# Performance work log

Hardware: AMD Instinct MI355X
Metric: run time of the kernel (lower is better)

## Reference

```python
import jax, jax.numpy as jnp
import numpy as np


def _gskan_layer(x, Lam, eps, a):
    # x: [B, n_in], Lam: [n_in, n_out], eps: [n_out], a: scalar PReLU weight
    s = x[:, :, None] + eps  # [B, n_in, n_out] broadcast add
    act = jnp.where(s >= 0, s, a * s)  # PReLU with single shared parameter
    return jnp.einsum('bpq,pq->bq', act, Lam)  # weighted sum over n_in


def setup_inputs() -> dict:
    key = jax.random.key(0)
    B, input_dim, width, depth, output_dim = 1024, 256, 512, 3, 256
    dims = [input_dim] + [width] * depth + [output_dim]
    ks = jax.random.split(key, 1 + 2 * (len(dims) - 1))
    inp = {"x": jax.random.normal(ks[0], (B, input_dim), dtype=jnp.float32)}
    for i in range(len(dims) - 1):
        n_in, n_out = dims[i], dims[i + 1]
        inp[f"L{i}_Lambda"] = 0.02 * jax.random.normal(ks[1 + 2 * i], (n_in, n_out), dtype=jnp.float32)
        inp[f"L{i}_eps"] = 0.02 * jax.random.normal(ks[2 + 2 * i], (n_out,), dtype=jnp.float32)
        inp[f"L{i}_a"] = jnp.float32(0.25)  # PReLU default init
    return inp


def reference(x,
              L0_Lambda, L0_eps, L0_a,
              L1_Lambda, L1_eps, L1_a,
              L2_Lambda, L2_eps, L2_a,
              L3_Lambda, L3_eps, L3_a):
    params = [(L0_Lambda, L0_eps, L0_a), (L1_Lambda, L1_eps, L1_a),
              (L2_Lambda, L2_eps, L2_a), (L3_Lambda, L3_eps, L3_a)]
    for Lam, eps, a in params:
        x = _gskan_layer(x, Lam, eps, a)
    return x
```

## Files before the change

### kernel.cpp

```cpp
#include <hip/hip_runtime.h>


#define PCHUNK 32
#define XS_STRIDE 36

__global__ __launch_bounds__(256) void gskan_partial_kernel(
    const float* __restrict__ X,
    const float* __restrict__ Lam,
    const float* __restrict__ Eps,
    const float* __restrict__ Aw,
    float* __restrict__ Part,
    int B, int n_in, int n_out, int p_per_split)
{
    __shared__ float xs[64 * XS_STRIDE];
    __shared__ float ls[PCHUNK * 64];

    const int tid = threadIdx.x;
    const int qg  = tid & 15;
    const int bl  = tid >> 4;

    const int q0 = blockIdx.x * 64;
    const int b0 = blockIdx.y * 64;
    const int p_begin = blockIdx.z * p_per_split;
    int p_end = p_begin + p_per_split;
    if (p_end > n_in) p_end = n_in;

    const float a  = Aw[0];
    const float c1 = 0.5f * (1.0f + a);
    const float c2 = 0.5f * (1.0f - a);

    const float4 ev = *reinterpret_cast<const float4*>(Eps + q0 + qg * 4);
    const float ee[4] = {ev.x, ev.y, ev.z, ev.w};

    float acc1[4][4] = {};
    float acc2[4][4] = {};

    for (int pc = p_begin; pc < p_end; pc += PCHUNK) {
        #pragma unroll
        for (int r = 0; r < 2; ++r) {
            int slot = r * 256 + tid;
            int row  = slot >> 3;
            int pg   = slot & 7;
            float4 v = *reinterpret_cast<const float4*>(
                X + (size_t)(b0 + row) * n_in + pc + pg * 4);
            *reinterpret_cast<float4*>(&xs[row * XS_STRIDE + pg * 4]) = v;
        }
        #pragma unroll
        for (int r = 0; r < 2; ++r) {
            int slot = r * 256 + tid;
            int row  = slot >> 4;
            int c4   = slot & 15;
            float4 v = *reinterpret_cast<const float4*>(
                Lam + (size_t)(pc + row) * n_out + q0 + c4 * 4);
            *reinterpret_cast<float4*>(&ls[row * 64 + c4 * 4]) = v;
        }
        __syncthreads();

        #pragma unroll
        for (int p = 0; p < PCHUNK; p += 4) {
            float4 xv[4];
            #pragma unroll
            for (int i = 0; i < 4; ++i)
                xv[i] = *reinterpret_cast<const float4*>(&xs[(bl * 4 + i) * XS_STRIDE + p]);

            #pragma unroll
            for (int pp = 0; pp < 4; ++pp) {
                float4 lv = *reinterpret_cast<const float4*>(&ls[(p + pp) * 64 + qg * 4]);
                const float le[4] = {lv.x, lv.y, lv.z, lv.w};
                #pragma unroll
                for (int i = 0; i < 4; ++i) {
                    const float xe = (pp == 0) ? xv[i].x :
                                     (pp == 1) ? xv[i].y :
                                     (pp == 2) ? xv[i].z : xv[i].w;
                    #pragma unroll
                    for (int j = 0; j < 4; ++j) {
                        const float s = xe + ee[j];
                        acc1[i][j] = fmaf(s,        le[j], acc1[i][j]);
                        acc2[i][j] = fmaf(fabsf(s), le[j], acc2[i][j]);
                    }
                }
            }
        }
        __syncthreads();
    }

    float* P = Part + (size_t)blockIdx.z * B * n_out;
    #pragma unroll
    for (int i = 0; i < 4; ++i) {
        const int b = b0 + bl * 4 + i;
        float4 o;
        o.x = c1 * acc1[i][0] + c2 * acc2[i][0];
        o.y = c1 * acc1[i][1] + c2 * acc2[i][1];
        o.z = c1 * acc1[i][2] + c2 * acc2[i][2];
        o.w = c1 * acc1[i][3] + c2 * acc2[i][3];
        *reinterpret_cast<float4*>(P + (size_t)b * n_out + q0 + qg * 4) = o;
    }
}

__global__ __launch_bounds__(256) void gskan_combine_kernel(
    const float* __restrict__ Part, float* __restrict__ Y, int n, int nsplit)
{
    int i = (blockIdx.x * 256 + threadIdx.x) * 4;
    if (i >= n) return;
    float4 acc = *reinterpret_cast<const float4*>(Part + i);
    for (int s = 1; s < nsplit; ++s) {
        float4 v = *reinterpret_cast<const float4*>(Part + (size_t)s * n + i);
        acc.x += v.x; acc.y += v.y; acc.z += v.z; acc.w += v.w;
    }
    *reinterpret_cast<float4*>(Y + i) = acc;
}

extern "C" void kernel_launch(void* const* d_in, const int* in_sizes, int n_in_args,
                              void* d_out, int out_size, void* d_ws, size_t ws_size,
                              hipStream_t stream)
{
    (void)n_in_args; (void)out_size;

    const float* x = (const float*)d_in[0];

    struct LayerP { const float *Lam, *Eps, *Aw; int n_in, n_out; };
    LayerP layers[4];
    for (int i = 0; i < 4; ++i) {
        layers[i].Lam   = (const float*)d_in[1 + 3 * i];
        layers[i].Eps   = (const float*)d_in[2 + 3 * i];
        layers[i].Aw    = (const float*)d_in[3 + 3 * i];
        layers[i].n_out = in_sizes[2 + 3 * i];
        layers[i].n_in  = in_sizes[1 + 3 * i] / layers[i].n_out;
    }
    const int B = in_sizes[0] / layers[0].n_in;

    char* ws = (char*)d_ws;
    float* Part = (float*)ws;
    float* yA   = (float*)(ws + (size_t)(16u << 20));
    float* yB   = (float*)(ws + (size_t)(18u << 20));
    const bool have_ws = ws_size >= (size_t)(20u << 20);

    const float* cur = x;
    for (int i = 0; i < 4; ++i) {
        const LayerP& ly = layers[i];
        const int nq = ly.n_out / 64;
        const int nb = B / 64;

        int nsplit = 1;
        if (have_ws) {
            nsplit = 1024 / (nq * nb);
            if (nsplit < 1) nsplit = 1;
            int max_split = ly.n_in / PCHUNK;
            if (nsplit > max_split) nsplit = max_split;
        }
        int p_per = ((ly.n_in + nsplit * PCHUNK - 1) / (nsplit * PCHUNK)) * PCHUNK;
        nsplit = (ly.n_in + p_per - 1) / p_per;

        while ((size_t)nsplit * B * ly.n_out * 4 > ((size_t)16u << 20)) nsplit--;
        if (nsplit < 1) nsplit = 1;
        p_per = ((ly.n_in + nsplit * PCHUNK - 1) / (nsplit * PCHUNK)) * PCHUNK;
        nsplit = (ly.n_in + p_per - 1) / p_per;

        float* Y = (i == 3) ? (float*)d_out : ((i % 2 == 0) ? yA : yB);
        float* dst = (nsplit == 1) ? Y : Part;

        dim3 grid(nq, nb, nsplit), block(256);
        hipLaunchKernelGGL(gskan_partial_kernel, grid, block, 0, stream,
                           cur, ly.Lam, ly.Eps, ly.Aw, dst,
                           B, ly.n_in, ly.n_out, p_per);

        if (nsplit > 1) {
            const int n = B * ly.n_out;
            dim3 cg((n / 4 + 255) / 256), cb(256);
            hipLaunchKernelGGL(gskan_combine_kernel, cg, cb, 0, stream, Part, Y, n, nsplit);
        }
        cur = Y;
    }
}
```

Baseline: 117.4 us.

## Replace split-K partial+combine with single-pass in-block K split and double buffering

Drops the global split-K scheme, which wrote partial sums to workspace and ran a separate combine kernel per layer. Each 512-thread block now splits n_in between two halves that reduce through shared memory, uses narrower output tiles (32 or 16 columns) to keep enough blocks in flight, and double-buffers the X/Lambda tiles with register prefetch. This removes the extra launches and the partial-sum memory traffic. In exchange each thread has less reuse per loaded value (fewer columns per thread), and the one-column variant leaves half the threads idle when loading Lambda.

```diff
diff --git a/kernel.cpp b/kernel.cpp
--- a/kernel.cpp
+++ b/kernel.cpp
@@ -4,117 +4,170 @@
 #define PCHUNK 32
 #define XS_STRIDE 36
 
-__global__ __launch_bounds__(256) void gskan_partial_kernel(
+template<int QPER>
+__global__ __launch_bounds__(512, 2) void gskan_layer_kernel(
     const float* __restrict__ X,
     const float* __restrict__ Lam,
     const float* __restrict__ Eps,
     const float* __restrict__ Aw,
-    float* __restrict__ Part,
-    int B, int n_in, int n_out, int p_per_split)
+    float* __restrict__ Y,
+    int B, int n_in, int n_out, int NB)
 {
-    __shared__ float xs[64 * XS_STRIDE];
-    __shared__ float ls[PCHUNK * 64];
-
-    const int tid = threadIdx.x;
-    const int qg  = tid & 15;
-    const int bl  = tid >> 4;
-
-    const int q0 = blockIdx.x * 64;
-    const int b0 = blockIdx.y * 64;
-    const int p_begin = blockIdx.z * p_per_split;
-    int p_end = p_begin + p_per_split;
-    if (p_end > n_in) p_end = n_in;
+    constexpr int QTILE = 16 * QPER;
+    __shared__ float xs[2][2][64 * XS_STRIDE];
+    __shared__ float ls[2][2][PCHUNK * QTILE];
+    __shared__ float red[64 * (QTILE + 1)];
+
+    const int tid  = threadIdx.x;
+    const int half = tid >> 8;
+    const int t    = tid & 255;
+    const int qg   = t & 15;
+    const int bl   = t >> 4;
+
+    const int b_tile = blockIdx.x % NB;
+    const int q_tile = blockIdx.x / NB;
+    const int b0 = b_tile * 64;
+    const int q0 = q_tile * QTILE;
 
     const float a  = Aw[0];
     const float c1 = 0.5f * (1.0f + a);
     const float c2 = 0.5f * (1.0f - a);
 
-    const float4 ev = *reinterpret_cast<const float4*>(Eps + q0 + qg * 4);
-    const float ee[4] = {ev.x, ev.y, ev.z, ev.w};
-
-    float acc1[4][4] = {};
-    float acc2[4][4] = {};
-
-    for (int pc = p_begin; pc < p_end; pc += PCHUNK) {
-        #pragma unroll
-        for (int r = 0; r < 2; ++r) {
-            int slot = r * 256 + tid;
-            int row  = slot >> 3;
-            int pg   = slot & 7;
-            float4 v = *reinterpret_cast<const float4*>(
-                X + (size_t)(b0 + row) * n_in + pc + pg * 4);
-            *reinterpret_cast<float4*>(&xs[row * XS_STRIDE + pg * 4]) = v;
-        }
-        #pragma unroll
-        for (int r = 0; r < 2; ++r) {
-            int slot = r * 256 + tid;
-            int row  = slot >> 4;
-            int c4   = slot & 15;
-            float4 v = *reinterpret_cast<const float4*>(
-                Lam + (size_t)(pc + row) * n_out + q0 + c4 * 4);
-            *reinterpret_cast<float4*>(&ls[row * 64 + c4 * 4]) = v;
-        }
-        __syncthreads();
-
+    float ee[QPER];
+    #pragma unroll
+    for (int j = 0; j < QPER; ++j) ee[j] = Eps[q0 + qg * QPER + j];
+
+    const int pbase  = half * (n_in >> 1);
+    const int nchunk = (n_in >> 1) / PCHUNK;
+
+    const int  xrow = t >> 3, xpg = t & 7;
+    const int  lrow = (QPER == 2) ? (t >> 3) : (t >> 2);
+    const int  lc4  = (QPER == 2) ? (t & 7)  : (t & 3);
+    const bool lact = (QPER == 2) ? true : (t < 128);
+
+    float (*xsb)[64 * XS_STRIDE] = xs[half];
+    float (*lsb)[PCHUNK * QTILE] = ls[half];
+
+    {
+        const int pc = pbase;
+        float4 v0 = *reinterpret_cast<const float4*>(
+            X + (size_t)(b0 + xrow) * n_in + pc + xpg * 4);
+        float4 v1 = *reinterpret_cast<const float4*>(
+            X + (size_t)(b0 + xrow + 32) * n_in + pc + xpg * 4);
+        *reinterpret_cast<float4*>(&xsb[0][xrow * XS_STRIDE + xpg * 4]) = v0;
+        *reinterpret_cast<float4*>(&xsb[0][(xrow + 32) * XS_STRIDE + xpg * 4]) = v1;
+        if (lact) {
+            float4 lv = *reinterpret_cast<const float4*>(
+                Lam + (size_t)(pc + lrow) * n_out + q0 + lc4 * 4);
+            *reinterpret_cast<float4*>(&lsb[0][lrow * QTILE + lc4 * 4]) = lv;
+        }
+    }
+    __syncthreads();
+
+    float acc1[4][QPER] = {};
+    float acc2[4][QPER] = {};
+
+    for (int c = 0; c < nchunk; ++c) {
+        const int cur = c & 1;
+        const bool hasnext = (c + 1 < nchunk);
+        float4 nx0, nx1, nl;
+        if (hasnext) {
+            const int pc = pbase + (c + 1) * PCHUNK;
+            nx0 = *reinterpret_cast<const float4*>(
+                X + (size_t)(b0 + xrow) * n_in + pc + xpg * 4);
+            nx1 = *reinterpret_cast<const float4*>(
+                X + (size_t)(b0 + xrow + 32) * n_in + pc + xpg * 4);
+            if (lact)
+                nl = *reinterpret_cast<const float4*>(
+                    Lam + (size_t)(pc + lrow) * n_out + q0 + lc4 * 4);
+        }
+
+        const float* xcur = xsb[cur];
+        const float* lcur = lsb[cur];
         #pragma unroll
         for (int p = 0; p < PCHUNK; p += 4) {
             float4 xv[4];
             #pragma unroll
             for (int i = 0; i < 4; ++i)
-                xv[i] = *reinterpret_cast<const float4*>(&xs[(bl * 4 + i) * XS_STRIDE + p]);
-
+                xv[i] = *reinterpret_cast<const float4*>(
+                    &xcur[(bl * 4 + i) * XS_STRIDE + p]);
+
+            float lvv[4][QPER];
             #pragma unroll
             for (int pp = 0; pp < 4; ++pp) {
-                float4 lv = *reinterpret_cast<const float4*>(&ls[(p + pp) * 64 + qg * 4]);
-                const float le[4] = {lv.x, lv.y, lv.z, lv.w};
+                if (QPER == 2) {
+                    float2 lw = *reinterpret_cast<const float2*>(
+                        &lcur[(p + pp) * QTILE + qg * 2]);
+                    lvv[pp][0] = lw.x; lvv[pp][1] = lw.y;
+                } else {
+                    lvv[pp][0] = lcur[(p + pp) * QTILE + qg];
+                }
+            }
+
+            #pragma unroll
+            for (int pp = 0; pp < 4; ++pp) {
                 #pragma unroll
                 for (int i = 0; i < 4; ++i) {
                     const float xe = (pp == 0) ? xv[i].x :
                                      (pp == 1) ? xv[i].y :
                                      (pp == 2) ? xv[i].z : xv[i].w;
                     #pragma unroll
-                    for (int j = 0; j < 4; ++j) {
+                    for (int j = 0; j < QPER; ++j) {
                         const float s = xe + ee[j];
-                        acc1[i][j] = fmaf(s,        le[j], acc1[i][j]);
-                        acc2[i][j] = fmaf(fabsf(s), le[j], acc2[i][j]);
+                        acc1[i][j] = fmaf(s,        lvv[pp][j], acc1[i][j]);
+                        acc2[i][j] = fmaf(fabsf(s), lvv[pp][j], acc2[i][j]);
                     }
                 }
             }
         }
+
+        if (hasnext) {
+            const int nxt = cur ^ 1;
+            *reinterpret_cast<float4*>(&xsb[nxt][xrow * XS_STRIDE + xpg * 4]) = nx0;
+            *reinterpret_cast<float4*>(&xsb[nxt][(xrow + 32) * XS_STRIDE + xpg * 4]) = nx1;
+            if (lact)
+                *reinterpret_cast<float4*>(&lsb[nxt][lrow * QTILE + lc4 * 4]) = nl;
+        }
         __syncthreads();
     }
 
-    float* P = Part + (size_t)blockIdx.z * B * n_out;
+    float o[4][QPER];
     #pragma unroll
-    for (int i = 0; i < 4; ++i) {
-        const int b = b0 + bl * 4 + i;
-        float4 o;
-        o.x = c1 * acc1[i][0] + c2 * acc2[i][0];
-        o.y = c1 * acc1[i][1] + c2 * acc2[i][1];
-        o.z = c1 * acc1[i][2] + c2 * acc2[i][2];
-        o.w = c1 * acc1[i][3] + c2 * acc2[i][3];
-        *reinterpret_cast<float4*>(P + (size_t)b * n_out + q0 + qg * 4) = o;
-    }
-}
-
-__global__ __launch_bounds__(256) void gskan_combine_kernel(
-    const float* __restrict__ Part, float* __restrict__ Y, int n, int nsplit)
-{
-    int i = (blockIdx.x * 256 + threadIdx.x) * 4;
-    if (i >= n) return;
-    float4 acc = *reinterpret_cast<const float4*>(Part + i);
-    for (int s = 1; s < nsplit; ++s) {
-        float4 v = *reinterpret_cast<const float4*>(Part + (size_t)s * n + i);
-        acc.x += v.x; acc.y += v.y; acc.z += v.z; acc.w += v.w;
-    }
-    *reinterpret_cast<float4*>(Y + i) = acc;
+    for (int i = 0; i < 4; ++i)
+        #pragma unroll
+        for (int j = 0; j < QPER; ++j)
+            o[i][j] = c1 * acc1[i][j] + c2 * acc2[i][j];
+
+    if (half == 1) {
+        #pragma unroll
+        for (int i = 0; i < 4; ++i)
+            #pragma unroll
+            for (int j = 0; j < QPER; ++j)
+                red[(bl * 4 + i) * (QTILE + 1) + qg * QPER + j] = o[i][j];
+    }
+    __syncthreads();
+    if (half == 0) {
+        #pragma unroll
+        for (int i = 0; i < 4; ++i) {
+            #pragma unroll
+            for (int j = 0; j < QPER; ++j)
+                o[i][j] += red[(bl * 4 + i) * (QTILE + 1) + qg * QPER + j];
+            float* dst = Y + (size_t)(b0 + bl * 4 + i) * n_out + q0 + qg * QPER;
+            if (QPER == 2) {
+                float2 st; st.x = o[i][0]; st.y = o[i][1];
+                *reinterpret_cast<float2*>(dst) = st;
+            } else {
+                dst[0] = o[i][0];
+            }
+        }
+    }
 }
 
 extern "C" void kernel_launch(void* const* d_in, const int* in_sizes, int n_in_args,
                               void* d_out, int out_size, void* d_ws, size_t ws_size,
                               hipStream_t stream)
 {
-    (void)n_in_args; (void)out_size;
+    (void)n_in_args; (void)out_size; (void)ws_size;
 
     const float* x = (const float*)d_in[0];
 
@@ -127,47 +180,26 @@
         layers[i].n_out = in_sizes[2 + 3 * i];
         layers[i].n_in  = in_sizes[1 + 3 * i] / layers[i].n_out;
     }
-    const int B = in_sizes[0] / layers[0].n_in;
+    const int B  = in_sizes[0] / layers[0].n_in;
+    const int NB = B / 64;
 
     char* ws = (char*)d_ws;
-    float* Part = (float*)ws;
-    float* yA   = (float*)(ws + (size_t)(16u << 20));
-    float* yB   = (float*)(ws + (size_t)(18u << 20));
-    const bool have_ws = ws_size >= (size_t)(20u << 20);
+    float* yA = (float*)ws;
+    float* yB = (float*)(ws + (size_t)(4u << 20));
 
     const float* cur = x;
     for (int i = 0; i < 4; ++i) {
         const LayerP& ly = layers[i];
-        const int nq = ly.n_out / 64;
-        const int nb = B / 64;
-
-        int nsplit = 1;
-        if (have_ws) {
-            nsplit = 1024 / (nq * nb);
-            if (nsplit < 1) nsplit = 1;
-            int max_split = ly.n_in / PCHUNK;
-            if (nsplit > max_split) nsplit = max_split;
-        }
-        int p_per = ((ly.n_in + nsplit * PCHUNK - 1) / (nsplit * PCHUNK)) * PCHUNK;
-        nsplit = (ly.n_in + p_per - 1) / p_per;
-
-        while ((size_t)nsplit * B * ly.n_out * 4 > ((size_t)16u << 20)) nsplit--;
-        if (nsplit < 1) nsplit = 1;
-        p_per = ((ly.n_in + nsplit * PCHUNK - 1) / (nsplit * PCHUNK)) * PCHUNK;
-        nsplit = (ly.n_in + p_per - 1) / p_per;
-
         float* Y = (i == 3) ? (float*)d_out : ((i % 2 == 0) ? yA : yB);
-        float* dst = (nsplit == 1) ? Y : Part;
-
-        dim3 grid(nq, nb, nsplit), block(256);
-        hipLaunchKernelGGL(gskan_partial_kernel, grid, block, 0, stream,
-                           cur, ly.Lam, ly.Eps, ly.Aw, dst,
-                           B, ly.n_in, ly.n_out, p_per);
-
-        if (nsplit > 1) {
-            const int n = B * ly.n_out;
-            dim3 cg((n / 4 + 255) / 256), cb(256);
-            hipLaunchKernelGGL(gskan_combine_kernel, cg, cb, 0, stream, Part, Y, n, nsplit);
+
+        if (ly.n_out >= 512) {
+            dim3 grid((ly.n_out / 32) * NB), block(512);
+            hipLaunchKernelGGL((gskan_layer_kernel<2>), grid, block, 0, stream,
+                               cur, ly.Lam, ly.Eps, ly.Aw, Y, B, ly.n_in, ly.n_out, NB);
+        } else {
+            dim3 grid((ly.n_out / 16) * NB), block(512);
+            hipLaunchKernelGGL((gskan_layer_kernel<1>), grid, block, 0, stream,
+                               cur, ly.Lam, ly.Eps, ly.Aw, Y, B, ly.n_in, ly.n_out, NB);
         }
         cur = Y;
     }
```

Measured after the change: 229.0 us. 95.0% more time.
